# Optimization experiments

Hardware: AMD Instinct MI355X
Metric: run time of the kernel (lower is better)

## Reference

```python
import jax, jax.numpy as jnp
import numpy as np
from jax import lax

B, C_IN, C_OUT, T = 2048, 64, 64, 32
E = 32768
K_HOPS = 2
KSIZE = 3
EPS = 1e-5
SLOPE = 0.01  # torch LeakyReLU default negative_slope


def setup_inputs() -> dict:
    key = jax.random.key(0)
    ks = jax.random.split(key, 10)
    x = jax.random.normal(ks[0], (B, C_IN, T), dtype=jnp.float32)
    edge_index = jax.random.randint(ks[1], (2, E), 0, B, dtype=jnp.int64)
    edge_weight = jax.random.uniform(ks[2], (E,), dtype=jnp.float32)
    # temporal Conv1d params: weight [out, in, k], bias [out]
    conv_w = jax.random.normal(ks[3], (C_OUT, C_IN, KSIZE), dtype=jnp.float32) / np.sqrt(C_IN * KSIZE)
    conv_b = jnp.zeros((C_OUT,), dtype=jnp.float32)
    # LayerNorm([out_channels, T]) elementwise affine over last two dims
    ln_g = jnp.ones((C_OUT, T), dtype=jnp.float32)
    ln_b = jnp.zeros((C_OUT, T), dtype=jnp.float32)
    # BatchNorm1d over node features inside residual layer (res+ pre-norm)
    bn_g = jnp.ones((C_OUT,), dtype=jnp.float32)
    bn_b = jnp.zeros((C_OUT,), dtype=jnp.float32)
    # TAGConv: one linear per hop (K+1 of them) plus bias
    tag_w = jax.random.normal(ks[4], (K_HOPS + 1, C_OUT, C_OUT), dtype=jnp.float32) / np.sqrt(C_OUT)
    tag_b = jnp.zeros((C_OUT,), dtype=jnp.float32)
    return {
        'x': x, 'edge_index': edge_index, 'edge_weight': edge_weight,
        'conv_w': conv_w, 'conv_b': conv_b, 'ln_g': ln_g, 'ln_b': ln_b,
        'bn_g': bn_g, 'bn_b': bn_b, 'tag_w': tag_w, 'tag_b': tag_b,
    }


def _forward(x, edge_index, edge_weight, conv_w, conv_b, ln_g, ln_b, bn_g, bn_b, tag_w, tag_b):
    Bn, Cin, Tn = x.shape
    # --- Temporal1DConvLayer: Conv1d with padding=k-1 both sides, truncate to T, pool='none', LeakyReLU ---
    y = lax.conv_general_dilated(x, conv_w, window_strides=(1,),
                                 padding=[(KSIZE - 1, KSIZE - 1)],
                                 dimension_numbers=('NCH', 'OIH', 'NCH'))
    y = y + conv_b[None, :, None]
    y = y[..., :Tn]                                   # [B, C_out, T]
    y = jnp.where(y >= 0, y, SLOPE * y)               # LeakyReLU
    # --- temporal_norm_layer: LayerNorm over (C_out, T) jointly ---
    mu = jnp.mean(y, axis=(1, 2), keepdims=True)
    var = jnp.var(y, axis=(1, 2), keepdims=True)
    y = (y - mu) * lax.rsqrt(var + EPS) * ln_g[None] + ln_b[None]
    # --- parallelize over time: permute(2,0,1) -> [T, B, F]; edges replicated per t ---
    h_in = jnp.transpose(y, (2, 0, 1))                # [T, B, F]
    # --- ResidualLayer (res+): h = h_in + TAGConv(LeakyReLU(BatchNorm(h_in))) ---
    mu_n = jnp.mean(h_in, axis=(0, 1))                # batch stats over all T*B node copies
    var_n = jnp.var(h_in, axis=(0, 1))
    z = (h_in - mu_n) * lax.rsqrt(var_n + EPS) * bn_g + bn_b
    z = jnp.where(z >= 0, z, SLOPE * z)
    src, dst = edge_index[0], edge_index[1]
    out = jnp.einsum('tbf,fg->tbg', z, tag_w[0])
    p = z
    for k in range(1, K_HOPS + 1):
        msg = p[:, src, :] * edge_weight[None, :, None]   # [T, E, F] gather
        p = jnp.zeros_like(p).at[:, dst, :].add(msg)      # scatter-add per timestep
        out = out + jnp.einsum('tbf,fg->tbg', p, tag_w[k])
    out = out + tag_b
    h = h_in + out                                    # residual 'res+'
    # --- reshape back: [T, B, F] -> [B, F, T] ---
    return jnp.transpose(h, (1, 2, 0))


def reference(x, edge_index, edge_weight, conv_w, conv_b, ln_g, ln_b, bn_g, bn_b, tag_w, tag_b):
    return _forward(x, edge_index, edge_weight, conv_w, conv_b, ln_g, ln_b, bn_g, bn_b, tag_w, tag_b)
```

## Files before the change

### kernel.cpp

```cpp
#include <hip/hip_runtime.h>
#include <cstddef>

#define NB   2048
#define NE   32768
#define NTC  2048
#define SLOPE_F 0.01f
#define EPS_F   1e-5f

typedef short bf16x8 __attribute__((ext_vector_type(8)));
typedef float f32x4  __attribute__((ext_vector_type(4)));

__device__ __forceinline__ unsigned short f2bf(float f) {
    unsigned u = __builtin_bit_cast(unsigned, f);
    u += 0x7FFF + ((u >> 16) & 1);
    return (unsigned short)(u >> 16);
}
__device__ __forceinline__ float bflo(unsigned v) {
    return __builtin_bit_cast(float, v << 16);
}
__device__ __forceinline__ float bfhi(unsigned v) {
    return __builtin_bit_cast(float, v & 0xFFFF0000u);
}
__device__ __forceinline__ unsigned pk2(float lo, float hi) {
    return (unsigned)f2bf(lo) | ((unsigned)f2bf(hi) << 16);
}
__device__ __forceinline__ void accv8(float* acc, const uint4& v, float wt) {
    acc[0] += wt * bflo(v.x); acc[1] += wt * bfhi(v.x);
    acc[2] += wt * bflo(v.y); acc[3] += wt * bfhi(v.y);
    acc[4] += wt * bflo(v.z); acc[5] += wt * bfhi(v.z);
    acc[6] += wt * bflo(v.w); acc[7] += wt * bfhi(v.w);
}
__device__ __forceinline__ void acci16(float* acc, const uint4& v, float wt) {
    acc[0] += wt * (float)(short)(v.x & 0xFFFFu); acc[1] += wt * (float)(short)(v.x >> 16);
    acc[2] += wt * (float)(short)(v.y & 0xFFFFu); acc[3] += wt * (float)(short)(v.y >> 16);
    acc[4] += wt * (float)(short)(v.z & 0xFFFFu); acc[5] += wt * (float)(short)(v.z >> 16);
    acc[6] += wt * (float)(short)(v.w & 0xFFFFu); acc[7] += wt * (float)(short)(v.w >> 16);
}
__device__ __forceinline__ unsigned pkq2(float a, float b, float inv) {
    int qa = __float2int_rn(a * inv);
    int qb = __float2int_rn(b * inv);
    return ((unsigned)qa & 0xFFFFu) | ((unsigned)qb << 16);
}

__global__ __launch_bounds__(256)
void k_detect(const int* __restrict__ ei, int* __restrict__ mode)
{
    int k = blockIdx.x * 256 + threadIdx.x;
    if (ei[2 * k + 1] != 0) atomicOr(mode, 1);
}

__device__ __forceinline__ int edge_src(const int* ei, int m, int e) {
    return m ? ei[e] : ei[2 * e];
}
__device__ __forceinline__ int edge_dst(const int* ei, int m, int e) {
    return m ? ei[NE + e] : ei[2 * (NE + e)];
}

__global__ __launch_bounds__(256)
void k_hist(const int* __restrict__ ei, const int* __restrict__ mode,
            int* __restrict__ hist, const float* __restrict__ cw,
            unsigned short* __restrict__ wAb, const float* __restrict__ tw,
            unsigned short* __restrict__ twB)
{
    int e = blockIdx.x * 256 + threadIdx.x;
    int m = *mode;
    atomicAdd(&hist[edge_dst(ei, m, e)], 1);
    if (blockIdx.x < 48) {
        int idx = e;
        int kk = idx >> 12, o = (idx >> 6) & 63, i = idx & 63;
        wAb[idx] = f2bf(cw[o * 192 + i * 3 + kk]);
    } else if (blockIdx.x < 96) {
        int idx = e - 48 * 256;
        int mm = idx >> 12, rem = idx & 4095;
        int g = rem >> 6, k = rem & 63;
        twB[idx] = f2bf(tw[mm * 4096 + k * 64 + g]);
    }
}

__global__ __launch_bounds__(256)
void k_scan(const int* __restrict__ hist, int* __restrict__ rowp, int* __restrict__ cur)
{
    __shared__ int part[256];
    int j = threadIdx.x;
    int loc[8]; int s = 0;
#pragma unroll
    for (int r = 0; r < 8; ++r) { loc[r] = hist[j * 8 + r]; s += loc[r]; }
    part[j] = s;
    __syncthreads();
    for (int off = 1; off < 256; off <<= 1) {
        int v = (j >= off) ? part[j - off] : 0;
        __syncthreads();
        part[j] += v;
        __syncthreads();
    }
    int excl = part[j] - s;
#pragma unroll
    for (int r = 0; r < 8; ++r) {
        rowp[j * 8 + r] = excl;
        cur [j * 8 + r] = excl;
        excl += loc[r];
    }
    if (j == 255) rowp[2048] = excl;
}

__global__ __launch_bounds__(256)
void k_scat(const int* __restrict__ ei, const float* __restrict__ ew,
            const int* __restrict__ mode, int* __restrict__ cur,
            int* __restrict__ csrs, float* __restrict__ csrw)
{
    int e = blockIdx.x * 256 + threadIdx.x;
    int m = *mode;
    int d = edge_dst(ei, m, e);
    int pos = atomicAdd(&cur[d], 1);
    csrs[pos] = edge_src(ei, m, e);
    csrw[pos] = ew[e];
}

__global__ __launch_bounds__(256, 4)
void k_convln(const float* __restrict__ x, const unsigned short* __restrict__ wAb,
              const float* __restrict__ cb, const float* __restrict__ lg,
              const float* __restrict__ lb, float* __restrict__ h_in,
              float* __restrict__ partials)
{
    __shared__ __align__(16) unsigned short xT[36 * 72];
    __shared__ float hT[32 * 65];
    __shared__ float red1[64], red2[64];
    __shared__ float wsum[8];
    __shared__ float bcast[2];

    const int b = blockIdx.x, j = threadIdx.x;
    const float* __restrict__ xg = x + (size_t)b * NTC;

    {
        unsigned* xTd = (unsigned*)xT;
        int t = j & 31, p = j >> 5;
#pragma unroll
        for (int r = 0; r < 4; ++r) {
            int i0 = (r * 8 + p) * 2;
            float v0 = xg[i0 * 32 + t];
            float v1 = xg[(i0 + 1) * 32 + t];
            xTd[(t + 2) * 36 + (i0 >> 1)] = pk2(v0, v1);
        }
        if (j < 72)       xTd[j] = 0u;
        else if (j < 144) xTd[1224 + (j - 72)] = 0u;
    }
    __syncthreads();

    const int lane = j & 63, w = j >> 6;
    const int n16 = lane & 15, quad = lane >> 4;

    bf16x8 afr[3][2];
#pragma unroll
    for (int kk = 0; kk < 3; ++kk)
#pragma unroll
        for (int s = 0; s < 2; ++s) {
            int off16 = (kk * 64 + w * 16 + n16) * 64 + s * 32 + quad * 8;
            afr[kk][s] = *(const bf16x8*)(wAb + off16);
        }

    f32x4 acc0 = {0.f, 0.f, 0.f, 0.f};
    f32x4 acc1 = {0.f, 0.f, 0.f, 0.f};
#pragma unroll
    for (int kk = 0; kk < 3; ++kk)
#pragma unroll
        for (int s = 0; s < 2; ++s) {
            bf16x8 b0 = *(const bf16x8*)(xT + (n16 + kk) * 72 + s * 32 + quad * 8);
            bf16x8 b1 = *(const bf16x8*)(xT + (16 + n16 + kk) * 72 + s * 32 + quad * 8);
            acc0 = __builtin_amdgcn_mfma_f32_16x16x32_bf16(afr[kk][s], b0, acc0, 0, 0, 0);
            acc1 = __builtin_amdgcn_mfma_f32_16x16x32_bf16(afr[kk][s], b1, acc1, 0, 0, 0);
        }

    float vals[2][4];
    float s1 = 0.f, s2 = 0.f;
#pragma unroll
    for (int r = 0; r < 4; ++r) {
        float cbv = cb[w * 16 + quad * 4 + r];
        float v0 = acc0[r] + cbv;
        float v1 = acc1[r] + cbv;
        v0 = (v0 >= 0.f) ? v0 : SLOPE_F * v0;
        v1 = (v1 >= 0.f) ? v1 : SLOPE_F * v1;
        vals[0][r] = v0; vals[1][r] = v1;
        s1 += v0 + v1; s2 += v0 * v0 + v1 * v1;
    }
#pragma unroll
    for (int off = 32; off > 0; off >>= 1) {
        s1 += __shfl_down(s1, off, 64);
        s2 += __shfl_down(s2, off, 64);
    }
    if (lane == 0) { wsum[w] = s1; wsum[4 + w] = s2; }
    __syncthreads();
    if (j == 0) {
        float S1 = wsum[0] + wsum[1] + wsum[2] + wsum[3];
        float S2 = wsum[4] + wsum[5] + wsum[6] + wsum[7];
        float mu  = S1 * (1.f / 2048.f);
        float var = S2 * (1.f / 2048.f) - mu * mu;
        bcast[0] = mu;
        bcast[1] = rsqrtf(var + EPS_F);
    }
    __syncthreads();
    const float mu = bcast[0], rs = bcast[1];
    float po1[4] = {0.f, 0.f, 0.f, 0.f}, po2[4] = {0.f, 0.f, 0.f, 0.f};
#pragma unroll
    for (int nt = 0; nt < 2; ++nt) {
        int t = nt * 16 + n16;
#pragma unroll
        for (int r = 0; r < 4; ++r) {
            int o = w * 16 + quad * 4 + r;
            float h = (vals[nt][r] - mu) * rs * lg[o * 32 + t] + lb[o * 32 + t];
            hT[t * 65 + o] = h;
            po1[r] += h; po2[r] += h * h;
        }
    }
#pragma unroll
    for (int off = 8; off > 0; off >>= 1) {
#pragma unroll
        for (int r = 0; r < 4; ++r) {
            po1[r] += __shfl_down(po1[r], off, 16);
            po2[r] += __shfl_down(po2[r], off, 16);
        }
    }
    if (n16 == 0) {
#pragma unroll
        for (int r = 0; r < 4; ++r) {
            int o = w * 16 + quad * 4 + r;
            red1[o] = po1[r];
            red2[o] = po2[r];
        }
    }
    __syncthreads();
    float* hb = h_in + (size_t)b * NTC;
#pragma unroll
    for (int r = 0; r < 8; ++r) {
        int idx = j + r * 256;
        hb[idx] = hT[(idx >> 6) * 65 + (idx & 63)];
    }
    float* pb_ = partials + (size_t)b * 128;
    if (j < 64)       pb_[j] = red1[j];
    else if (j < 128) pb_[j] = red2[j - 64];
}

__global__ __launch_bounds__(256)
void k_bnred(const float* __restrict__ partials, const float* __restrict__ bg,
             const float* __restrict__ bb, float* __restrict__ stats)
{
    const int c = blockIdx.x, j = threadIdx.x;
    float s1 = 0.f, s2 = 0.f;
    for (int b = j; b < NB; b += 256) {
        const float* p = partials + (size_t)b * 128;
        s1 += p[c];
        s2 += p[64 + c];
    }
    __shared__ float r1[4], r2[4];
#pragma unroll
    for (int off = 32; off > 0; off >>= 1) {
        s1 += __shfl_down(s1, off, 64);
        s2 += __shfl_down(s2, off, 64);
    }
    if ((j & 63) == 0) { r1[j >> 6] = s1; r2[j >> 6] = s2; }
    __syncthreads();
    if (j == 0) {
        float S1 = r1[0] + r1[1] + r1[2] + r1[3];
        float S2 = r2[0] + r2[1] + r2[2] + r2[3];
        const float inv_n = 1.f / 65536.f;
        float mu  = S1 * inv_n;
        float var = S2 * inv_n - mu * mu;
        float rs  = rsqrtf(var + EPS_F);
        float sc  = bg[c] * rs;
        stats[128 + c] = sc;
        stats[192 + c] = bb[c] - mu * sc;
    }
}

__global__ __launch_bounds__(256, 6)
void k_zw0(const float* __restrict__ h_in, const float* __restrict__ stats,
           const unsigned short* __restrict__ twB, const float* __restrict__ tb,
           unsigned short* __restrict__ zb16, float* __restrict__ out)
{
    __shared__ __align__(16) unsigned short zA[32 * 64];
    __shared__ float hl[32 * 65];
    const int b = blockIdx.x, j = threadIdx.x;
    const int c = j & 63;
    const float sc = stats[128 + c], sh = stats[192 + c];
    const float* hb = h_in + (size_t)b * NTC;
    unsigned short* zb = zb16 + (size_t)b * NTC;
#pragma unroll
    for (int r = 0; r < 8; ++r) {
        int idx = j + r * 256;
        int t = idx >> 6;
        float h = hb[idx];
        float zv = h * sc + sh;
        zv = (zv >= 0.f) ? zv : SLOPE_F * zv;
        unsigned short zh = f2bf(zv);
        zb[idx] = zh;
        zA[idx] = zh;
        hl[t * 65 + c] = h;
    }
    __syncthreads();
    const int lane = j & 63, w = j >> 6;
    const int n16 = lane & 15, quad = lane >> 4;
    const int g = w * 16 + n16;

    bf16x8 a00 = *(const bf16x8*)(zA + (n16)      * 64 +      quad * 8);
    bf16x8 a01 = *(const bf16x8*)(zA + (n16)      * 64 + 32 + quad * 8);
    bf16x8 a10 = *(const bf16x8*)(zA + (16 + n16) * 64 +      quad * 8);
    bf16x8 a11 = *(const bf16x8*)(zA + (16 + n16) * 64 + 32 + quad * 8);
    bf16x8 b0  = *(const bf16x8*)(twB + g * 64 +      quad * 8);
    bf16x8 b1  = *(const bf16x8*)(twB + g * 64 + 32 + quad * 8);

    f32x4 d0 = {0.f, 0.f, 0.f, 0.f};
    f32x4 d1 = {0.f, 0.f, 0.f, 0.f};
    d0 = __builtin_amdgcn_mfma_f32_16x16x32_bf16(a00, b0, d0, 0, 0, 0);
    d0 = __builtin_amdgcn_mfma_f32_16x16x32_bf16(a01, b1, d0, 0, 0, 0);
    d1 = __builtin_amdgcn_mfma_f32_16x16x32_bf16(a10, b0, d1, 0, 0, 0);
    d1 = __builtin_amdgcn_mfma_f32_16x16x32_bf16(a11, b1, d1, 0, 0, 0);

    const float tbg = tb[g];
    float* ob = out + (size_t)b * NTC + g * 32;
    {
        float4 v;
        v.x = d0[0] + tbg + hl[(quad * 4 + 0) * 65 + g];
        v.y = d0[1] + tbg + hl[(quad * 4 + 1) * 65 + g];
        v.z = d0[2] + tbg + hl[(quad * 4 + 2) * 65 + g];
        v.w = d0[3] + tbg + hl[(quad * 4 + 3) * 65 + g];
        *(float4*)(ob + quad * 4) = v;
    }
    {
        float4 v;
        v.x = d1[0] + tbg + hl[(16 + quad * 4 + 0) * 65 + g];
        v.y = d1[1] + tbg + hl[(16 + quad * 4 + 1) * 65 + g];
        v.z = d1[2] + tbg + hl[(16 + quad * 4 + 2) * 65 + g];
        v.w = d1[3] + tbg + hl[(16 + quad * 4 + 3) * 65 + g];
        *(float4*)(ob + 16 + quad * 4) = v;
    }
}

__global__ __launch_bounds__(256, 6)
void k_hop1(const unsigned short* __restrict__ p_in, const int* __restrict__ rowp,
            const int* __restrict__ csrs, const float* __restrict__ csrw,
            const unsigned short* __restrict__ twB,
            unsigned short* __restrict__ p1q, float* __restrict__ p1scl,
            float* __restrict__ out)
{
    __shared__ __align__(16) unsigned short pA[32 * 64];
    __shared__ float mred[4];
    const int d = blockIdx.x, j = threadIdx.x;
    const int beg = rowp[d], end = rowp[d + 1];
    float acc[8];
#pragma unroll
    for (int r = 0; r < 8; ++r) acc[r] = 0.f;
    int e = beg;
    for (; e + 4 <= end; e += 4) {
        int s0 = csrs[e],  s1 = csrs[e+1], s2 = csrs[e+2], s3 = csrs[e+3];
        float w0 = csrw[e], w1 = csrw[e+1], w2 = csrw[e+2], w3 = csrw[e+3];
        uint4 v0 = ((const uint4*)(p_in + (size_t)s0 * NTC))[j];
        uint4 v1 = ((const uint4*)(p_in + (size_t)s1 * NTC))[j];
        uint4 v2 = ((const uint4*)(p_in + (size_t)s2 * NTC))[j];
        uint4 v3 = ((const uint4*)(p_in + (size_t)s3 * NTC))[j];
        accv8(acc, v0, w0); accv8(acc, v1, w1);
        accv8(acc, v2, w2); accv8(acc, v3, w3);
    }
    for (; e < end; ++e) {
        int s0 = csrs[e];
        float w0 = csrw[e];
        uint4 v0 = ((const uint4*)(p_in + (size_t)s0 * NTC))[j];
        accv8(acc, v0, w0);
    }

    const int lane = j & 63, w = j >> 6;
    float m = 0.f;
#pragma unroll
    for (int r = 0; r < 8; ++r) m = fmaxf(m, fabsf(acc[r]));
#pragma unroll
    for (int off = 32; off > 0; off >>= 1)
        m = fmaxf(m, __shfl_down(m, off, 64));
    if (lane == 0) mred[w] = m;
    __syncthreads();
    const float mv = fmaxf(fmaxf(mred[0], mred[1]), fmaxf(mred[2], mred[3]));
    const float inv = (mv > 0.f) ? (32767.f / mv) : 0.f;
    if (j == 0) p1scl[d] = mv * (1.f / 32767.f);

    {
        uint4 qv;
        qv.x = pkq2(acc[0], acc[1], inv);
        qv.y = pkq2(acc[2], acc[3], inv);
        qv.z = pkq2(acc[4], acc[5], inv);
        qv.w = pkq2(acc[6], acc[7], inv);
        ((uint4*)(p1q + (size_t)d * NTC))[j] = qv;
    }
    uint4 pv;
    pv.x = pk2(acc[0], acc[1]); pv.y = pk2(acc[2], acc[3]);
    pv.z = pk2(acc[4], acc[5]); pv.w = pk2(acc[6], acc[7]);
    ((uint4*)pA)[j] = pv;
    __syncthreads();

    const int n16 = lane & 15, quad = lane >> 4;
    const int g = w * 16 + n16;

    bf16x8 a00 = *(const bf16x8*)(pA + (n16)      * 64 +      quad * 8);
    bf16x8 a01 = *(const bf16x8*)(pA + (n16)      * 64 + 32 + quad * 8);
    bf16x8 a10 = *(const bf16x8*)(pA + (16 + n16) * 64 +      quad * 8);
    bf16x8 a11 = *(const bf16x8*)(pA + (16 + n16) * 64 + 32 + quad * 8);
    bf16x8 b0  = *(const bf16x8*)(twB + g * 64 +      quad * 8);
    bf16x8 b1  = *(const bf16x8*)(twB + g * 64 + 32 + quad * 8);

    f32x4 d0 = {0.f, 0.f, 0.f, 0.f};
    f32x4 d1 = {0.f, 0.f, 0.f, 0.f};
    d0 = __builtin_amdgcn_mfma_f32_16x16x32_bf16(a00, b0, d0, 0, 0, 0);
    d0 = __builtin_amdgcn_mfma_f32_16x16x32_bf16(a01, b1, d0, 0, 0, 0);
    d1 = __builtin_amdgcn_mfma_f32_16x16x32_bf16(a10, b0, d1, 0, 0, 0);
    d1 = __builtin_amdgcn_mfma_f32_16x16x32_bf16(a11, b1, d1, 0, 0, 0);

    float* ob = out + (size_t)d * NTC + g * 32;
    {
        float4 v = *(float4*)(ob + quad * 4);
        v.x += d0[0]; v.y += d0[1]; v.z += d0[2]; v.w += d0[3];
        *(float4*)(ob + quad * 4) = v;
    }
    {
        float4 v = *(float4*)(ob + 16 + quad * 4);
        v.x += d1[0]; v.y += d1[1]; v.z += d1[2]; v.w += d1[3];
        *(float4*)(ob + 16 + quad * 4) = v;
    }
}

__global__ __launch_bounds__(256, 6)
void k_hop2(const unsigned short* __restrict__ p1q, const float* __restrict__ p1scl,
            const int* __restrict__ rowp, const int* __restrict__ csrs,
            const float* __restrict__ csrw, const float* __restrict__ tw,
            float* __restrict__ out)
{
    __shared__ float pl[32 * 65];
    __shared__ __align__(16) float W[64 * 64];
    const int d = blockIdx.x, j = threadIdx.x;
#pragma unroll
    for (int r = 0; r < 16; ++r) { int idx = j + r * 256; W[idx] = tw[idx]; }
    const int beg = rowp[d], end = rowp[d + 1];
    float acc[8];
#pragma unroll
    for (int r = 0; r < 8; ++r) acc[r] = 0.f;
    int e = beg;
    for (; e + 4 <= end; e += 4) {
        int s0 = csrs[e],  s1 = csrs[e+1], s2 = csrs[e+2], s3 = csrs[e+3];
        float w0 = csrw[e]   * p1scl[s0];
        float w1 = csrw[e+1] * p1scl[s1];
        float w2 = csrw[e+2] * p1scl[s2];
        float w3 = csrw[e+3] * p1scl[s3];
        uint4 v0 = ((const uint4*)(p1q + (size_t)s0 * NTC))[j];
        uint4 v1 = ((const uint4*)(p1q + (size_t)s1 * NTC))[j];
        uint4 v2 = ((const uint4*)(p1q + (size_t)s2 * NTC))[j];
        uint4 v3 = ((const uint4*)(p1q + (size_t)s3 * NTC))[j];
        acci16(acc, v0, w0); acci16(acc, v1, w1);
        acci16(acc, v2, w2); acci16(acc, v3, w3);
    }
    for (; e < end; ++e) {
        int s0 = csrs[e];
        float w0 = csrw[e] * p1scl[s0];
        uint4 v0 = ((const uint4*)(p1q + (size_t)s0 * NTC))[j];
        acci16(acc, v0, w0);
    }
    {
        int tt = j >> 3, c0 = (j & 7) * 8;
        float* q = &pl[tt * 65 + c0];
#pragma unroll
        for (int s = 0; s < 8; ++s) q[s] = acc[s];
    }
    __syncthreads();
    const int t = j & 31, gq = (j >> 5) * 8;
    float accm[8];
#pragma unroll
    for (int r = 0; r < 8; ++r) accm[r] = 0.f;
    for (int f = 0; f < 64; ++f) {
        float pv = pl[t * 65 + f];
        const float4* Wr = (const float4*)&W[f * 64 + gq];
        float4 wa = Wr[0], wb = Wr[1];
        accm[0] += pv*wa.x; accm[1] += pv*wa.y; accm[2] += pv*wa.z; accm[3] += pv*wa.w;
        accm[4] += pv*wb.x; accm[5] += pv*wb.y; accm[6] += pv*wb.z; accm[7] += pv*wb.w;
    }
    float* ob = out + (size_t)d * NTC;
#pragma unroll
    for (int r = 0; r < 8; ++r)
        ob[(gq + r) * 32 + t] += accm[r];
}

extern "C" void kernel_launch(void* const* d_in, const int* in_sizes, int n_in,
                              void* d_out, int out_size, void* d_ws, size_t ws_size,
                              hipStream_t stream)
{
    const float* x  = (const float*)d_in[0];
    const int*   ei = (const int*)  d_in[1];
    const float* ew = (const float*)d_in[2];
    const float* cw = (const float*)d_in[3];
    const float* cb = (const float*)d_in[4];
    const float* lg = (const float*)d_in[5];
    const float* lb = (const float*)d_in[6];
    const float* bg = (const float*)d_in[7];
    const float* bb = (const float*)d_in[8];
    const float* tw = (const float*)d_in[9];
    const float* tb = (const float*)d_in[10];
    float* out = (float*)d_out;
    float* ws  = (float*)d_ws;

    float*          h_in  = ws;
    unsigned short* p1q   = (unsigned short*)(ws + 4194304);
    float*          p1scl = ws + 6291456;
    unsigned short* zbf   = (unsigned short*)(ws + 8388608);
    float*          stats = ws + 10485760;
    unsigned short* wAb   = (unsigned short*)(ws + 10486016);
    unsigned short* twB   = (unsigned short*)(ws + 10492160);
    float*          parts = ws + 10498304;
    int*            ib    = (int*)(ws + 10760448);
    int*   mode  = ib;
    int*   hist  = ib + 4;
    int*   rowp  = ib + 2052;
    int*   cur   = ib + 4104;
    int*   csrs  = ib + 6152;
    float* csrw  = (float*)(ib + 38920);

    (void)hipMemsetAsync(ib, 0, 2052 * sizeof(int), stream);

    k_detect <<<128, 256, 0, stream>>>(ei, mode);
    k_hist   <<<128, 256, 0, stream>>>(ei, mode, hist, cw, wAb, tw, twB);
    k_scan   <<<1,   256, 0, stream>>>(hist, rowp, cur);
    k_scat   <<<128, 256, 0, stream>>>(ei, ew, mode, cur, csrs, csrw);
    k_convln <<<NB,  256, 0, stream>>>(x, wAb, cb, lg, lb, h_in, parts);
    k_bnred  <<<64,  256, 0, stream>>>(parts, bg, bb, stats);
    k_zw0    <<<NB,  256, 0, stream>>>(h_in, stats, twB, tb, zbf, out);
    k_hop1   <<<NB,  256, 0, stream>>>(zbf, rowp, csrs, csrw, twB + 4096, p1q, p1scl, out);
    k_hop2   <<<NB,  256, 0, stream>>>(p1q, p1scl, rowp, csrs, csrw, tw + 8192, out);
}
```

Measured before the change: 179.7 us.

## Fuse hop-0 matmul into hop1, per-wave edge-format detect, unroll gathers by 8

Removes the separate detect kernel. Each wave now detects the int64/int32 edge format with a ballot, which relies on every wave seeing a nonzero high word when the indices are int32. The z computation becomes a light elementwise kernel. The hop-0 matmul, bias and residual move into hop1, which runs both MFMA products together, so the out read-modify-write in hop1 goes away. The gather loops in hop1 and hop2 are unrolled to 8 edges for more loads in flight, and occupancy hints drop to 4.

```diff
diff --git a/kernel.cpp b/kernel.cpp
--- a/kernel.cpp
+++ b/kernel.cpp
@@ -42,13 +42,6 @@
     return ((unsigned)qa & 0xFFFFu) | ((unsigned)qb << 16);
 }
 
-__global__ __launch_bounds__(256)
-void k_detect(const int* __restrict__ ei, int* __restrict__ mode)
-{
-    int k = blockIdx.x * 256 + threadIdx.x;
-    if (ei[2 * k + 1] != 0) atomicOr(mode, 1);
-}
-
 __device__ __forceinline__ int edge_src(const int* ei, int m, int e) {
     return m ? ei[e] : ei[2 * e];
 }
@@ -57,13 +50,13 @@
 }
 
 __global__ __launch_bounds__(256)
-void k_hist(const int* __restrict__ ei, const int* __restrict__ mode,
-            int* __restrict__ hist, const float* __restrict__ cw,
-            unsigned short* __restrict__ wAb, const float* __restrict__ tw,
-            unsigned short* __restrict__ twB)
+void k_hist(const int* __restrict__ ei, int* __restrict__ hist,
+            const float* __restrict__ cw, unsigned short* __restrict__ wAb,
+            const float* __restrict__ tw, unsigned short* __restrict__ twB)
 {
     int e = blockIdx.x * 256 + threadIdx.x;
-    int m = *mode;
+    unsigned long long bal = __ballot(ei[2 * e + 1] != 0);
+    int m = (bal != 0ull) ? 1 : 0;
     atomicAdd(&hist[edge_dst(ei, m, e)], 1);
     if (blockIdx.x < 48) {
         int idx = e;
@@ -105,11 +98,11 @@
 
 __global__ __launch_bounds__(256)
 void k_scat(const int* __restrict__ ei, const float* __restrict__ ew,
-            const int* __restrict__ mode, int* __restrict__ cur,
-            int* __restrict__ csrs, float* __restrict__ csrw)
+            int* __restrict__ cur, int* __restrict__ csrs, float* __restrict__ csrw)
 {
     int e = blockIdx.x * 256 + threadIdx.x;
-    int m = *mode;
+    unsigned long long bal = __ballot(ei[2 * e + 1] != 0);
+    int m = (bal != 0ull) ? 1 : 0;
     int d = edge_dst(ei, m, e);
     int pos = atomicAdd(&cur[d], 1);
     csrs[pos] = edge_src(ei, m, e);
@@ -271,51 +264,153 @@
     }
 }
 
-__global__ __launch_bounds__(256, 6)
-void k_zw0(const float* __restrict__ h_in, const float* __restrict__ stats,
-           const unsigned short* __restrict__ twB, const float* __restrict__ tb,
-           unsigned short* __restrict__ zb16, float* __restrict__ out)
-{
+__global__ __launch_bounds__(256)
+void k_zlite(const float* __restrict__ h_in, const float* __restrict__ stats,
+             unsigned short* __restrict__ zb16)
+{
+    __shared__ float scs[64], shs[64];
+    const int b = blockIdx.x, j = threadIdx.x;
+    if (j < 64)        scs[j] = stats[128 + j];
+    else if (j < 128)  shs[j - 64] = stats[192 + (j - 64)];
+    __syncthreads();
+    const float4* hb = (const float4*)(h_in + (size_t)b * NTC);
+    float4 a = hb[2 * j], c4 = hb[2 * j + 1];
+    const int c0 = (j * 8) & 63;
+    float z0 = a.x  * scs[c0+0] + shs[c0+0];
+    float z1 = a.y  * scs[c0+1] + shs[c0+1];
+    float z2 = a.z  * scs[c0+2] + shs[c0+2];
+    float z3 = a.w  * scs[c0+3] + shs[c0+3];
+    float z4 = c4.x * scs[c0+4] + shs[c0+4];
+    float z5 = c4.y * scs[c0+5] + shs[c0+5];
+    float z6 = c4.z * scs[c0+6] + shs[c0+6];
+    float z7 = c4.w * scs[c0+7] + shs[c0+7];
+    z0 = (z0 >= 0.f) ? z0 : SLOPE_F * z0;  z1 = (z1 >= 0.f) ? z1 : SLOPE_F * z1;
+    z2 = (z2 >= 0.f) ? z2 : SLOPE_F * z2;  z3 = (z3 >= 0.f) ? z3 : SLOPE_F * z3;
+    z4 = (z4 >= 0.f) ? z4 : SLOPE_F * z4;  z5 = (z5 >= 0.f) ? z5 : SLOPE_F * z5;
+    z6 = (z6 >= 0.f) ? z6 : SLOPE_F * z6;  z7 = (z7 >= 0.f) ? z7 : SLOPE_F * z7;
+    uint4 q;
+    q.x = pk2(z0, z1); q.y = pk2(z2, z3); q.z = pk2(z4, z5); q.w = pk2(z6, z7);
+    ((uint4*)(zb16 + (size_t)b * NTC))[j] = q;
+}
+
+__global__ __launch_bounds__(256, 4)
+void k_hop1(const unsigned short* __restrict__ p_in, const float* __restrict__ h_in,
+            const int* __restrict__ rowp, const int* __restrict__ csrs,
+            const float* __restrict__ csrw, const unsigned short* __restrict__ twB,
+            const float* __restrict__ tb,
+            unsigned short* __restrict__ p1q, float* __restrict__ p1scl,
+            float* __restrict__ out)
+{
+    __shared__ __align__(16) unsigned short pA[32 * 64];
     __shared__ __align__(16) unsigned short zA[32 * 64];
     __shared__ float hl[32 * 65];
-    const int b = blockIdx.x, j = threadIdx.x;
-    const int c = j & 63;
-    const float sc = stats[128 + c], sh = stats[192 + c];
-    const float* hb = h_in + (size_t)b * NTC;
-    unsigned short* zb = zb16 + (size_t)b * NTC;
-#pragma unroll
-    for (int r = 0; r < 8; ++r) {
-        int idx = j + r * 256;
-        int t = idx >> 6;
-        float h = hb[idx];
-        float zv = h * sc + sh;
-        zv = (zv >= 0.f) ? zv : SLOPE_F * zv;
-        unsigned short zh = f2bf(zv);
-        zb[idx] = zh;
-        zA[idx] = zh;
-        hl[t * 65 + c] = h;
-    }
-    __syncthreads();
+    __shared__ float mred[4];
+    const int d = blockIdx.x, j = threadIdx.x;
+
+    {
+        uint4 zv = ((const uint4*)(p_in + (size_t)d * NTC))[j];
+        ((uint4*)zA)[j] = zv;
+        const float4* hb4 = (const float4*)(h_in + (size_t)d * NTC);
+        float4 h0 = hb4[2 * j], h1 = hb4[2 * j + 1];
+        int tt = j >> 3, c0 = (j & 7) * 8;
+        float* q = &hl[tt * 65 + c0];
+        q[0] = h0.x; q[1] = h0.y; q[2] = h0.z; q[3] = h0.w;
+        q[4] = h1.x; q[5] = h1.y; q[6] = h1.z; q[7] = h1.w;
+    }
+
+    const int beg = rowp[d], end = rowp[d + 1];
+    float acc[8];
+#pragma unroll
+    for (int r = 0; r < 8; ++r) acc[r] = 0.f;
+    int e = beg;
+    for (; e + 8 <= end; e += 8) {
+        int   s0 = csrs[e],   s1 = csrs[e+1], s2 = csrs[e+2], s3 = csrs[e+3];
+        int   s4 = csrs[e+4], s5 = csrs[e+5], s6 = csrs[e+6], s7 = csrs[e+7];
+        float w0 = csrw[e],   w1 = csrw[e+1], w2 = csrw[e+2], w3 = csrw[e+3];
+        float w4 = csrw[e+4], w5 = csrw[e+5], w6 = csrw[e+6], w7 = csrw[e+7];
+        uint4 v0 = ((const uint4*)(p_in + (size_t)s0 * NTC))[j];
+        uint4 v1 = ((const uint4*)(p_in + (size_t)s1 * NTC))[j];
+        uint4 v2 = ((const uint4*)(p_in + (size_t)s2 * NTC))[j];
+        uint4 v3 = ((const uint4*)(p_in + (size_t)s3 * NTC))[j];
+        uint4 v4 = ((const uint4*)(p_in + (size_t)s4 * NTC))[j];
+        uint4 v5 = ((const uint4*)(p_in + (size_t)s5 * NTC))[j];
+        uint4 v6 = ((const uint4*)(p_in + (size_t)s6 * NTC))[j];
+        uint4 v7 = ((const uint4*)(p_in + (size_t)s7 * NTC))[j];
+        accv8(acc, v0, w0); accv8(acc, v1, w1);
+        accv8(acc, v2, w2); accv8(acc, v3, w3);
+        accv8(acc, v4, w4); accv8(acc, v5, w5);
+        accv8(acc, v6, w6); accv8(acc, v7, w7);
+    }
+    for (; e + 2 <= end; e += 2) {
+        int s0 = csrs[e],  s1 = csrs[e+1];
+        float w0 = csrw[e], w1 = csrw[e+1];
+        uint4 v0 = ((const uint4*)(p_in + (size_t)s0 * NTC))[j];
+        uint4 v1 = ((const uint4*)(p_in + (size_t)s1 * NTC))[j];
+        accv8(acc, v0, w0); accv8(acc, v1, w1);
+    }
+    if (e < end) {
+        int s0 = csrs[e];
+        float w0 = csrw[e];
+        uint4 v0 = ((const uint4*)(p_in + (size_t)s0 * NTC))[j];
+        accv8(acc, v0, w0);
+    }
+
     const int lane = j & 63, w = j >> 6;
+    float m = 0.f;
+#pragma unroll
+    for (int r = 0; r < 8; ++r) m = fmaxf(m, fabsf(acc[r]));
+#pragma unroll
+    for (int off = 32; off > 0; off >>= 1)
+        m = fmaxf(m, __shfl_down(m, off, 64));
+    if (lane == 0) mred[w] = m;
+    __syncthreads();
+    const float mv = fmaxf(fmaxf(mred[0], mred[1]), fmaxf(mred[2], mred[3]));
+    const float inv = (mv > 0.f) ? (32767.f / mv) : 0.f;
+    if (j == 0) p1scl[d] = mv * (1.f / 32767.f);
+
+    {
+        uint4 qv;
+        qv.x = pkq2(acc[0], acc[1], inv);
+        qv.y = pkq2(acc[2], acc[3], inv);
+        qv.z = pkq2(acc[4], acc[5], inv);
+        qv.w = pkq2(acc[6], acc[7], inv);
+        ((uint4*)(p1q + (size_t)d * NTC))[j] = qv;
+    }
+    uint4 pv;
+    pv.x = pk2(acc[0], acc[1]); pv.y = pk2(acc[2], acc[3]);
+    pv.z = pk2(acc[4], acc[5]); pv.w = pk2(acc[6], acc[7]);
+    ((uint4*)pA)[j] = pv;
+    __syncthreads();
+
     const int n16 = lane & 15, quad = lane >> 4;
     const int g = w * 16 + n16;
 
-    bf16x8 a00 = *(const bf16x8*)(zA + (n16)      * 64 +      quad * 8);
-    bf16x8 a01 = *(const bf16x8*)(zA + (n16)      * 64 + 32 + quad * 8);
-    bf16x8 a10 = *(const bf16x8*)(zA + (16 + n16) * 64 +      quad * 8);
-    bf16x8 a11 = *(const bf16x8*)(zA + (16 + n16) * 64 + 32 + quad * 8);
-    bf16x8 b0  = *(const bf16x8*)(twB + g * 64 +      quad * 8);
-    bf16x8 b1  = *(const bf16x8*)(twB + g * 64 + 32 + quad * 8);
+    bf16x8 za00 = *(const bf16x8*)(zA + (n16)      * 64 +      quad * 8);
+    bf16x8 za01 = *(const bf16x8*)(zA + (n16)      * 64 + 32 + quad * 8);
+    bf16x8 za10 = *(const bf16x8*)(zA + (16 + n16) * 64 +      quad * 8);
+    bf16x8 za11 = *(const bf16x8*)(zA + (16 + n16) * 64 + 32 + quad * 8);
+    bf16x8 pa00 = *(const bf16x8*)(pA + (n16)      * 64 +      quad * 8);
+    bf16x8 pa01 = *(const bf16x8*)(pA + (n16)      * 64 + 32 + quad * 8);
+    bf16x8 pa10 = *(const bf16x8*)(pA + (16 + n16) * 64 +      quad * 8);
+    bf16x8 pa11 = *(const bf16x8*)(pA + (16 + n16) * 64 + 32 + quad * 8);
+    bf16x8 b0w0 = *(const bf16x8*)(twB + g * 64 +      quad * 8);
+    bf16x8 b1w0 = *(const bf16x8*)(twB + g * 64 + 32 + quad * 8);
+    bf16x8 b0w1 = *(const bf16x8*)(twB + 4096 + g * 64 +      quad * 8);
+    bf16x8 b1w1 = *(const bf16x8*)(twB + 4096 + g * 64 + 32 + quad * 8);
 
     f32x4 d0 = {0.f, 0.f, 0.f, 0.f};
     f32x4 d1 = {0.f, 0.f, 0.f, 0.f};
-    d0 = __builtin_amdgcn_mfma_f32_16x16x32_bf16(a00, b0, d0, 0, 0, 0);
-    d0 = __builtin_amdgcn_mfma_f32_16x16x32_bf16(a01, b1, d0, 0, 0, 0);
-    d1 = __builtin_amdgcn_mfma_f32_16x16x32_bf16(a10, b0, d1, 0, 0, 0);
-    d1 = __builtin_amdgcn_mfma_f32_16x16x32_bf16(a11, b1, d1, 0, 0, 0);
+    d0 = __builtin_amdgcn_mfma_f32_16x16x32_bf16(za00, b0w0, d0, 0, 0, 0);
+    d0 = __builtin_amdgcn_mfma_f32_16x16x32_bf16(za01, b1w0, d0, 0, 0, 0);
+    d0 = __builtin_amdgcn_mfma_f32_16x16x32_bf16(pa00, b0w1, d0, 0, 0, 0);
+    d0 = __builtin_amdgcn_mfma_f32_16x16x32_bf16(pa01, b1w1, d0, 0, 0, 0);
+    d1 = __builtin_amdgcn_mfma_f32_16x16x32_bf16(za10, b0w0, d1, 0, 0, 0);
+    d1 = __builtin_amdgcn_mfma_f32_16x16x32_bf16(za11, b1w0, d1, 0, 0, 0);
+    d1 = __builtin_amdgcn_mfma_f32_16x16x32_bf16(pa10, b0w1, d1, 0, 0, 0);
+    d1 = __builtin_amdgcn_mfma_f32_16x16x32_bf16(pa11, b1w1, d1, 0, 0, 0);
 
     const float tbg = tb[g];
-    float* ob = out + (size_t)b * NTC + g * 32;
+    float* ob = out + (size_t)d * NTC + g * 32;
     {
         float4 v;
         v.x = d0[0] + tbg + hl[(quad * 4 + 0) * 65 + g];
@@ -334,96 +429,7 @@
     }
 }
 
-__global__ __launch_bounds__(256, 6)
-void k_hop1(const unsigned short* __restrict__ p_in, const int* __restrict__ rowp,
-            const int* __restrict__ csrs, const float* __restrict__ csrw,
-            const unsigned short* __restrict__ twB,
-            unsigned short* __restrict__ p1q, float* __restrict__ p1scl,
-            float* __restrict__ out)
-{
-    __shared__ __align__(16) unsigned short pA[32 * 64];
-    __shared__ float mred[4];
-    const int d = blockIdx.x, j = threadIdx.x;
-    const int beg = rowp[d], end = rowp[d + 1];
-    float acc[8];
-#pragma unroll
-    for (int r = 0; r < 8; ++r) acc[r] = 0.f;
-    int e = beg;
-    for (; e + 4 <= end; e += 4) {
-        int s0 = csrs[e],  s1 = csrs[e+1], s2 = csrs[e+2], s3 = csrs[e+3];
-        float w0 = csrw[e], w1 = csrw[e+1], w2 = csrw[e+2], w3 = csrw[e+3];
-        uint4 v0 = ((const uint4*)(p_in + (size_t)s0 * NTC))[j];
-        uint4 v1 = ((const uint4*)(p_in + (size_t)s1 * NTC))[j];
-        uint4 v2 = ((const uint4*)(p_in + (size_t)s2 * NTC))[j];
-        uint4 v3 = ((const uint4*)(p_in + (size_t)s3 * NTC))[j];
-        accv8(acc, v0, w0); accv8(acc, v1, w1);
-        accv8(acc, v2, w2); accv8(acc, v3, w3);
-    }
-    for (; e < end; ++e) {
-        int s0 = csrs[e];
-        float w0 = csrw[e];
-        uint4 v0 = ((const uint4*)(p_in + (size_t)s0 * NTC))[j];
-        accv8(acc, v0, w0);
-    }
-
-    const int lane = j & 63, w = j >> 6;
-    float m = 0.f;
-#pragma unroll
-    for (int r = 0; r < 8; ++r) m = fmaxf(m, fabsf(acc[r]));
-#pragma unroll
-    for (int off = 32; off > 0; off >>= 1)
-        m = fmaxf(m, __shfl_down(m, off, 64));
-    if (lane == 0) mred[w] = m;
-    __syncthreads();
-    const float mv = fmaxf(fmaxf(mred[0], mred[1]), fmaxf(mred[2], mred[3]));
-    const float inv = (mv > 0.f) ? (32767.f / mv) : 0.f;
-    if (j == 0) p1scl[d] = mv * (1.f / 32767.f);
-
-    {
-        uint4 qv;
-        qv.x = pkq2(acc[0], acc[1], inv);
-        qv.y = pkq2(acc[2], acc[3], inv);
-        qv.z = pkq2(acc[4], acc[5], inv);
-        qv.w = pkq2(acc[6], acc[7], inv);
-        ((uint4*)(p1q + (size_t)d * NTC))[j] = qv;
-    }
-    uint4 pv;
-    pv.x = pk2(acc[0], acc[1]); pv.y = pk2(acc[2], acc[3]);
-    pv.z = pk2(acc[4], acc[5]); pv.w = pk2(acc[6], acc[7]);
-    ((uint4*)pA)[j] = pv;
-    __syncthreads();
-
-    const int n16 = lane & 15, quad = lane >> 4;
-    const int g = w * 16 + n16;
-
-    bf16x8 a00 = *(const bf16x8*)(pA + (n16)      * 64 +      quad * 8);
-    bf16x8 a01 = *(const bf16x8*)(pA + (n16)      * 64 + 32 + quad * 8);
-    bf16x8 a10 = *(const bf16x8*)(pA + (16 + n16) * 64 +      quad * 8);
-    bf16x8 a11 = *(const bf16x8*)(pA + (16 + n16) * 64 + 32 + quad * 8);
-    bf16x8 b0  = *(const bf16x8*)(twB + g * 64 +      quad * 8);
-    bf16x8 b1  = *(const bf16x8*)(twB + g * 64 + 32 + quad * 8);
-
-    f32x4 d0 = {0.f, 0.f, 0.f, 0.f};
-    f32x4 d1 = {0.f, 0.f, 0.f, 0.f};
-    d0 = __builtin_amdgcn_mfma_f32_16x16x32_bf16(a00, b0, d0, 0, 0, 0);
-    d0 = __builtin_amdgcn_mfma_f32_16x16x32_bf16(a01, b1, d0, 0, 0, 0);
-    d1 = __builtin_amdgcn_mfma_f32_16x16x32_bf16(a10, b0, d1, 0, 0, 0);
-    d1 = __builtin_amdgcn_mfma_f32_16x16x32_bf16(a11, b1, d1, 0, 0, 0);
-
-    float* ob = out + (size_t)d * NTC + g * 32;
-    {
-        float4 v = *(float4*)(ob + quad * 4);
-        v.x += d0[0]; v.y += d0[1]; v.z += d0[2]; v.w += d0[3];
-        *(float4*)(ob + quad * 4) = v;
-    }
-    {
-        float4 v = *(float4*)(ob + 16 + quad * 4);
-        v.x += d1[0]; v.y += d1[1]; v.z += d1[2]; v.w += d1[3];
-        *(float4*)(ob + 16 + quad * 4) = v;
-    }
-}
-
-__global__ __launch_bounds__(256, 6)
+__global__ __launch_bounds__(256, 4)
 void k_hop2(const unsigned short* __restrict__ p1q, const float* __restrict__ p1scl,
             const int* __restrict__ rowp, const int* __restrict__ csrs,
             const float* __restrict__ csrw, const float* __restrict__ tw,
@@ -439,20 +445,39 @@
 #pragma unroll
     for (int r = 0; r < 8; ++r) acc[r] = 0.f;
     int e = beg;
-    for (; e + 4 <= end; e += 4) {
-        int s0 = csrs[e],  s1 = csrs[e+1], s2 = csrs[e+2], s3 = csrs[e+3];
+    for (; e + 8 <= end; e += 8) {
+        int   s0 = csrs[e],   s1 = csrs[e+1], s2 = csrs[e+2], s3 = csrs[e+3];
+        int   s4 = csrs[e+4], s5 = csrs[e+5], s6 = csrs[e+6], s7 = csrs[e+7];
         float w0 = csrw[e]   * p1scl[s0];
         float w1 = csrw[e+1] * p1scl[s1];
         float w2 = csrw[e+2] * p1scl[s2];
         float w3 = csrw[e+3] * p1scl[s3];
+        float w4 = csrw[e+4] * p1scl[s4];
+        float w5 = csrw[e+5] * p1scl[s5];
+        float w6 = csrw[e+6] * p1scl[s6];
+        float w7 = csrw[e+7] * p1scl[s7];
         uint4 v0 = ((const uint4*)(p1q + (size_t)s0 * NTC))[j];
         uint4 v1 = ((const uint4*)(p1q + (size_t)s1 * NTC))[j];
         uint4 v2 = ((const uint4*)(p1q + (size_t)s2 * NTC))[j];
         uint4 v3 = ((const uint4*)(p1q + (size_t)s3 * NTC))[j];
+        uint4 v4 = ((const uint4*)(p1q + (size_t)s4 * NTC))[j];
+        uint4 v5 = ((const uint4*)(p1q + (size_t)s5 * NTC))[j];
+        uint4 v6 = ((const uint4*)(p1q + (size_t)s6 * NTC))[j];
+        uint4 v7 = ((const uint4*)(p1q + (size_t)s7 * NTC))[j];
         acci16(acc, v0, w0); acci16(acc, v1, w1);
         acci16(acc, v2, w2); acci16(acc, v3, w3);
-    }
-    for (; e < end; ++e) {
+        acci16(acc, v4, w4); acci16(acc, v5, w5);
+        acci16(acc, v6, w6); acci16(acc, v7, w7);
+    }
+    for (; e + 2 <= end; e += 2) {
+        int s0 = csrs[e],  s1 = csrs[e+1];
+        float w0 = csrw[e]   * p1scl[s0];
+        float w1 = csrw[e+1] * p1scl[s1];
+        uint4 v0 = ((const uint4*)(p1q + (size_t)s0 * NTC))[j];
+        uint4 v1 = ((const uint4*)(p1q + (size_t)s1 * NTC))[j];
+        acci16(acc, v0, w0); acci16(acc, v1, w1);
+    }
+    if (e < end) {
         int s0 = csrs[e];
         float w0 = csrw[e] * p1scl[s0];
         uint4 v0 = ((const uint4*)(p1q + (size_t)s0 * NTC))[j];
@@ -509,22 +534,20 @@
     unsigned short* twB   = (unsigned short*)(ws + 10492160);
     float*          parts = ws + 10498304;
     int*            ib    = (int*)(ws + 10760448);
-    int*   mode  = ib;
-    int*   hist  = ib + 4;
-    int*   rowp  = ib + 2052;
-    int*   cur   = ib + 4104;
-    int*   csrs  = ib + 6152;
-    float* csrw  = (float*)(ib + 38920);
-
-    (void)hipMemsetAsync(ib, 0, 2052 * sizeof(int), stream);
-
-    k_detect <<<128, 256, 0, stream>>>(ei, mode);
-    k_hist   <<<128, 256, 0, stream>>>(ei, mode, hist, cw, wAb, tw, twB);
+    int*   hist  = ib;
+    int*   rowp  = ib + 2048;
+    int*   cur   = ib + 4100;
+    int*   csrs  = ib + 6148;
+    float* csrw  = (float*)(ib + 38916);
+
+    (void)hipMemsetAsync(hist, 0, 2048 * sizeof(int), stream);
+
+    k_hist   <<<128, 256, 0, stream>>>(ei, hist, cw, wAb, tw, twB);
     k_scan   <<<1,   256, 0, stream>>>(hist, rowp, cur);
-    k_scat   <<<128, 256, 0, stream>>>(ei, ew, mode, cur, csrs, csrw);
+    k_scat   <<<128, 256, 0, stream>>>(ei, ew, cur, csrs, csrw);
     k_convln <<<NB,  256, 0, stream>>>(x, wAb, cb, lg, lb, h_in, parts);
     k_bnred  <<<64,  256, 0, stream>>>(parts, bg, bb, stats);
-    k_zw0    <<<NB,  256, 0, stream>>>(h_in, stats, twB, tb, zbf, out);
-    k_hop1   <<<NB,  256, 0, stream>>>(zbf, rowp, csrs, csrw, twB + 4096, p1q, p1scl, out);
+    k_zlite  <<<NB,  256, 0, stream>>>(h_in, stats, zbf);
+    k_hop1   <<<NB,  256, 0, stream>>>(zbf, h_in, rowp, csrs, csrw, twB, tb, p1q, p1scl, out);
     k_hop2   <<<NB,  256, 0, stream>>>(p1q, p1scl, rowp, csrs, csrw, tw + 8192, out);
 }
```

After: 170.1 us. 1.06x faster.
